# Performance work log

Measured on AMD Instinct MI355X. Metric: run time of the kernel, lower is better.

Reference implementation:

```python
import jax, jax.numpy as jnp
import numpy as np

N_NEIGHBORS = 200
OUT_HW = 64

def avg_pool3(x):
    # F.avg_pool2d(x, 3, stride=1, padding=1), count_include_pad=True -> divide by 9
    s = jax.lax.reduce_window(x, 0.0, jax.lax.add, (1, 1, 3, 3), (1, 1, 1, 1),
                              ((0, 0), (0, 0), (1, 1), (1, 1)))
    return s / 9.0

def coord_conv1x1(x, w, b):
    # CoordConv2d: append normalized x/y coord channels in [-1,1], then 1x1 conv.
    B, C, H, W = x.shape
    yy = jnp.linspace(-1.0, 1.0, H, dtype=x.dtype)
    xx = jnp.linspace(-1.0, 1.0, W, dtype=x.dtype)
    xg = jnp.broadcast_to(xx[None, :], (H, W))
    yg = jnp.broadcast_to(yy[:, None], (H, W))
    coords = jnp.broadcast_to(jnp.stack([xg, yg])[None], (B, 2, H, W))
    xc = jnp.concatenate([x, coords], axis=1)  # (B, C+2, H, W)
    return jnp.einsum('bchw,oc->bohw', xc, w) + b[None, :, None, None]

def resize64(x):
    B, C, _, _ = x.shape
    return jax.image.resize(x, (B, C, OUT_HW, OUT_HW), method='bilinear')

def descriptor(p0, p1, p2, w1, b1, w2, b2, w3, b3):
    o1 = resize64(coord_conv1x1(avg_pool3(p0), w1, b1))
    o2 = resize64(coord_conv1x1(avg_pool3(p1), w2, b2))
    o3 = resize64(coord_conv1x1(avg_pool3(p2), w3, b3))
    return jnp.concatenate([o1, o2, o3], axis=1)  # (B, 1792, 64, 64)

def setup_inputs() -> dict:
    key = jax.random.key(0)
    ks = jax.random.split(key, 10)
    s = 0.05
    return {
        'p0': jax.random.normal(ks[0], (4, 256, 64, 64), jnp.float32),
        'p1': jax.random.normal(ks[1], (4, 512, 32, 32), jnp.float32),
        'p2': jax.random.normal(ks[2], (4, 1024, 16, 16), jnp.float32),
        'label': 0,
        'mask': jnp.ones((4, 1, 64, 64), jnp.float32),
        'w1': jax.random.normal(ks[3], (256, 258), jnp.float32) * s,
        'b1': jax.random.normal(ks[4], (256,), jnp.float32) * s,
        'w2': jax.random.normal(ks[5], (512, 514), jnp.float32) * s,
        'b2': jax.random.normal(ks[6], (512,), jnp.float32) * s,
        'w3': jax.random.normal(ks[7], (1024, 1026), jnp.float32) * s,
        'b3': jax.random.normal(ks[8], (1024,), jnp.float32) * s,
        'C': jax.random.normal(ks[9], (1792, 4096), jnp.float32),
    }

def reference(p0, p1, p2, label, mask, w1, b1, w2, b2, w3, b3, C):
    PHI_P = descriptor(p0, p1, p2, w1, b1, w2, b2, w3, b3)  # (B, 1792, 64, 64)
    B = PHI_P.shape[0]
    # b c h w -> b (h w) c
    phi_p = PHI_P.reshape(B, 1792, OUT_HW * OUT_HW).transpose(0, 2, 1)  # (B, 4096, 1792)
    feats = jnp.sum(phi_p * phi_p, axis=2, keepdims=True)       # (B, 4096, 1)
    cents = jnp.sum(C * C, axis=0, keepdims=True)                # (1, 4096)
    f_c = 2.0 * jnp.matmul(phi_p, C)                             # (B, 4096, 4096)
    dist = jnp.sqrt(feats + cents - f_c)
    # topk smallest: top_k on negated distances, sorted ascending after negation
    neg_vals, _ = jax.lax.top_k(-dist, N_NEIGHBORS)              # (B, 4096, 200)
    score = -neg_vals
    # b (h w) c -> b c h w
    score = score.reshape(B, OUT_HW, OUT_HW, N_NEIGHBORS).transpose(0, 3, 1, 2)
    return (score, PHI_P[:, :896, :, :])
```

## Files before the change

### kernel.cpp

```cpp
#include <hip/hip_runtime.h>
#include <hip/hip_bf16.h>
#include <hip/hip_fp8.h>
#include <stdint.h>

typedef unsigned short u16;
typedef __attribute__((ext_vector_type(8))) short bf16x8;
typedef __attribute__((ext_vector_type(4))) unsigned short u16x4;
typedef __attribute__((ext_vector_type(4))) float f32x4;
typedef __attribute__((ext_vector_type(2))) long lx2;

#define AS1 __attribute__((address_space(1)))
#define AS3 __attribute__((address_space(3)))

__device__ __forceinline__ u16 f2bf(float f) {
  uint32_t x = __float_as_uint(f);
  uint32_t r = (x + 0x7FFFu + ((x >> 16) & 1u)) >> 16;
  return (u16)r;
}
__device__ __forceinline__ float bf2f(u16 u) {
  return __uint_as_float(((uint32_t)u) << 16);
}
__device__ __forceinline__ uint8_t f2f8(float f) {
  __hip_fp8_e4m3 t(f);
  return (uint8_t)t.__x;
}
__device__ __forceinline__ float f82f(uint8_t v) {
  __hip_fp8_e4m3 t;
  t.__x = (__hip_fp8_storage_t)v;
  return (float)t;
}

__device__ __forceinline__ int permcol(int c) {
  return (c & ~63) | (((c >> 3) & 3) << 4) | (((c >> 5) & 1) << 3) | (c & 7);
}

__device__ __forceinline__ void gload_lds16(const void* g, void* l) {
  __builtin_amdgcn_global_load_lds((const AS1 void*)g, (AS3 void*)l, 16, 0, 0);
}

template <int C, int H, int W>
__global__ __launch_bounds__(256) void pool_trans(const float* __restrict__ in,
                                                  u16* __restrict__ PT) {
  constexpr int HW = H * W;
  int hwt = blockIdx.x, ct = blockIdx.y, b = blockIdx.z;
  int tid = threadIdx.x;
  __shared__ float t[32][33];
  {
    int c_l = tid >> 3;
    int hw_l = (tid & 7) * 4;
    int c = ct * 32 + c_l;
    int hw = hwt * 32 + hw_l;
    int y = hw / W;
    int x0 = hw % W;
    const float* pl = in + ((size_t)b * C + c) * HW;
    float cs[6] = {0, 0, 0, 0, 0, 0};
    #pragma unroll
    for (int dy = -1; dy <= 1; dy++) {
      int yy = y + dy;
      if ((unsigned)yy < (unsigned)H) {
        const float* row = pl + yy * W;
        #pragma unroll
        for (int k = 0; k < 6; k++) {
          int xx = x0 - 1 + k;
          if ((unsigned)xx < (unsigned)W) cs[k] += row[xx];
        }
      }
    }
    #pragma unroll
    for (int k = 0; k < 4; k++)
      t[c_l][hw_l + k] = (cs[k] + cs[k + 1] + cs[k + 2]) * (1.0f / 9.0f);
  }
  __syncthreads();
  int hw_w = tid >> 3;
  int c_w = (tid & 7) * 4;
  u16x4 o;
  #pragma unroll
  for (int j = 0; j < 4; j++) o[j] = f2bf(t[c_w + j][hw_w]);
  *(u16x4*)&PT[((size_t)b * HW + hwt * 32 + hw_w) * C + ct * 32 + c_w] = o;
}

__global__ void wconv_bf16(const float* __restrict__ wf, u16* __restrict__ wb,
                           int logk, int total) {
  int idx = blockIdx.x * 256 + threadIdx.x;
  if (idx >= total) return;
  int K = 1 << logk;
  int o = idx >> (logk - 3);
  int k0 = (idx & ((K >> 3) - 1)) * 8;
  const float* src = wf + (size_t)o * (K + 2) + k0;
  bf16x8 v;
  #pragma unroll
  for (int e = 0; e < 8; e++) v[e] = (short)f2bf(src[e]);
  *(bf16x8*)&wb[(size_t)o * K + k0] = v;
}

template <int K, int HW, int WD, int OC, int PHIC, int CST, bool OUT8>
__global__ __launch_bounds__(256) void conv_gemm(
    const u16* __restrict__ Wb,
    const u16* __restrict__ PT,
    const float* __restrict__ wf,
    const float* __restrict__ bias,
    float* __restrict__ outHW, size_t outHW_bstride,
    void* __restrict__ outCM) {
  constexpr int LOGW = (WD == 64) ? 6 : (WD == 32) ? 5 : 4;
  constexpr int LOGHW = 2 * LOGW;
  int n0 = blockIdx.x * 128, m0 = blockIdx.y * 128;
  int tid = threadIdx.x;
  int wid = tid >> 6, lane = tid & 63;
  int wm = wid >> 1, wn = wid & 1;
  __shared__ u16 As[128 * 64];
  __shared__ u16 Bs[128 * 64];
  f32x4 acc[4][4] = {};
  int lrow = tid >> 3;
  int lcol = (tid & 7) * 8;
  const u16* ga = Wb + (size_t)(m0 + lrow) * K + lcol;
  const u16* gb = PT + (size_t)(n0 + lrow) * K + lcol;
  char* lbaseA = (char*)As + wid * 1024;
  char* lbaseB = (char*)Bs + wid * 1024;
  for (int k0 = 0; k0 < K; k0 += 64) {
    #pragma unroll
    for (int q = 0; q < 4; q++) {
      gload_lds16(ga + (size_t)q * 32 * K + k0, lbaseA + q * 4096);
      gload_lds16(gb + (size_t)q * 32 * K + k0, lbaseB + q * 4096);
    }
    __syncthreads();
    #pragma unroll
    for (int kk = 0; kk < 2; kk++) {
      bf16x8 af[4], bfr[4];
      int kb = kk * 32 + (lane >> 4) * 8;
      #pragma unroll
      for (int i = 0; i < 4; i++)
        af[i] = *(const bf16x8*)&As[(wm * 64 + i * 16 + (lane & 15)) * 64 + kb];
      #pragma unroll
      for (int j = 0; j < 4; j++)
        bfr[j] = *(const bf16x8*)&Bs[(wn * 64 + j * 16 + (lane & 15)) * 64 + kb];
      #pragma unroll
      for (int i = 0; i < 4; i++)
        #pragma unroll
        for (int j = 0; j < 4; j++)
          acc[i][j] = __builtin_amdgcn_mfma_f32_16x16x32_bf16(af[i], bfr[j], acc[i][j], 0, 0, 0);
    }
    __syncthreads();
  }
  int rq = lane >> 4, cq = lane & 15;
  #pragma unroll
  for (int mi = 0; mi < 4; mi++) {
    int lm = m0 + wm * 64 + mi * 16 + rq * 4;
    float wxr[4], wyr[4], bbr[4];
    #pragma unroll
    for (int r = 0; r < 4; r++) {
      int o = lm + r;
      wxr[r] = wf[(size_t)o * (K + 2) + K];
      wyr[r] = wf[(size_t)o * (K + 2) + K + 1];
      bbr[r] = bias[o];
    }
    #pragma unroll
    for (int ni = 0; ni < 4; ni++) {
      int gn = n0 + wn * 64 + ni * 16 + cq;
      int b = gn >> LOGHW;
      int hw = gn & (HW - 1);
      int x = hw & (WD - 1), y = hw >> LOGW;
      float xg = -1.0f + x * (2.0f / (WD - 1));
      float yg = -1.0f + y * (2.0f / (WD - 1));
      float vals[4];
      #pragma unroll
      for (int r = 0; r < 4; r++)
        vals[r] = acc[mi][ni][r] + wxr[r] * xg + wyr[r] * yg + bbr[r];
      if (lm < PHIC) {
        #pragma unroll
        for (int r = 0; r < 4; r++)
          outHW[(size_t)b * outHW_bstride + (size_t)(lm + r) * HW + hw] = vals[r];
      }
      if constexpr (OUT8) {
        uint32_t pk = (uint32_t)f2f8(vals[0]) | ((uint32_t)f2f8(vals[1]) << 8) |
                      ((uint32_t)f2f8(vals[2]) << 16) | ((uint32_t)f2f8(vals[3]) << 24);
        *(uint32_t*)&((uint8_t*)outCM)[((size_t)b * HW + hw) * CST + permcol(lm)] = pk;
      } else {
        u16x4 pk;
        #pragma unroll
        for (int r = 0; r < 4; r++) pk[r] = f2bf(vals[r]);
        *(u16x4*)&((u16*)outCM)[((size_t)b * HW + hw) * CST + lm] = pk;
      }
    }
  }
}

template <int Hin>
__device__ __forceinline__ void bilin_coords(int v, int& i0, int& i1, float& wgt) {
  constexpr float scale = (float)Hin / 64.0f;
  float f = ((float)v + 0.5f) * scale - 0.5f;
  float f0 = floorf(f);
  wgt = f - f0;
  int i = (int)f0;
  i1 = min(i + 1, Hin - 1);
  i0 = max(i, 0);
}

template <int C, int Cin, int Hin>
__global__ void emit_phi_v(const float* __restrict__ in, float* __restrict__ outp,
                           int ch_off) {
  int idx = blockIdx.x * 256 + threadIdx.x;
  int x0 = (idx & 15) * 4;
  int y = (idx >> 4) & 63;
  int c = (idx >> 10) % C;
  int b = idx / (C * 1024);
  const float* pl = in + (size_t)(b * Cin + c) * (Hin * Hin);
  int y0, y1; float wy;
  bilin_coords<Hin>(y, y0, y1, wy);
  const float* r0 = pl + y0 * Hin;
  const float* r1 = pl + y1 * Hin;
  f32x4 o;
  #pragma unroll
  for (int k = 0; k < 4; k++) {
    int xx0, xx1; float wx;
    bilin_coords<Hin>(x0 + k, xx0, xx1, wx);
    float top = (1.0f - wx) * r0[xx0] + wx * r0[xx1];
    float bot = (1.0f - wx) * r1[xx0] + wx * r1[xx1];
    o[k] = (1.0f - wy) * top + wy * bot;
  }
  *(f32x4*)&outp[((size_t)b * 896 + ch_off + c) * 4096 + (y << 6) + x0] = o;
}

__global__ __launch_bounds__(256) void trans_f32_fp8(
    const float* __restrict__ in, uint8_t* __restrict__ outT, int R, int Cc, int OS) {
  int r0 = blockIdx.y * 32, c0 = blockIdx.x * 32;
  __shared__ float t[32][33];
  int tid = threadIdx.x;
  int cl = tid & 31, rl = tid >> 5;
  #pragma unroll
  for (int q = 0; q < 4; q++)
    t[rl + q * 8][cl] = in[(size_t)(r0 + rl + q * 8) * Cc + c0 + cl];
  __syncthreads();
  #pragma unroll
  for (int q = 0; q < 4; q++) {
    int c = c0 + rl + q * 8;
    outT[(size_t)c * OS + permcol(r0 + cl)] = f2f8(t[cl][rl + q * 8]);
  }
}

template <int C, int Hin, int L>
__global__ void gather_A(const u16* __restrict__ OT, uint8_t* __restrict__ A,
                         int ch_off) {
  int idx = blockIdx.x * 256 + threadIdx.x;
  int co = (idx & ((C / 8) - 1)) * 8;
  int hw = (idx >> L) & 4095;
  int b = idx >> (L + 12);
  int x = hw & 63, y = hw >> 6;
  int y0, y1, x0, x1; float wy, wx;
  bilin_coords<Hin>(y, y0, y1, wy);
  bilin_coords<Hin>(x, x0, x1, wx);
  float w00 = (1.0f - wy) * (1.0f - wx), w01 = (1.0f - wy) * wx;
  float w10 = wy * (1.0f - wx), w11 = wy * wx;
  const u16* base = OT + (size_t)b * (Hin * Hin) * C + co;
  bf16x8 t00 = *(const bf16x8*)&base[(y0 * Hin + x0) * C];
  bf16x8 t01 = *(const bf16x8*)&base[(y0 * Hin + x1) * C];
  bf16x8 t10 = *(const bf16x8*)&base[(y1 * Hin + x0) * C];
  bf16x8 t11 = *(const bf16x8*)&base[(y1 * Hin + x1) * C];
  uint32_t pk[2] = {0, 0};
  #pragma unroll
  for (int e = 0; e < 8; e++) {
    float v = w00 * bf2f((u16)t00[e]) + w01 * bf2f((u16)t01[e]) +
              w10 * bf2f((u16)t10[e]) + w11 * bf2f((u16)t11[e]);
    pk[e >> 2] |= ((uint32_t)f2f8(v)) << ((e & 3) * 8);
  }
  uint2 o; o.x = pk[0]; o.y = pk[1];
  *(uint2*)&A[((size_t)b * 4096 + hw) * 1792 + permcol(ch_off + co)] = o;
}

__global__ __launch_bounds__(256) void rownorm8(const uint8_t* __restrict__ X,
                                                float* __restrict__ out, int ncols) {
  int row = blockIdx.x * 4 + (threadIdx.x >> 6);
  int lane = threadIdx.x & 63;
  const uint8_t* xr = X + (size_t)row * ncols;
  int n8 = ncols >> 3;
  float s = 0.0f;
  for (int c8 = lane; c8 < n8; c8 += 64) {
    uint2 v = *(const uint2*)&xr[c8 * 8];
    #pragma unroll
    for (int e = 0; e < 4; e++) {
      float f = f82f((uint8_t)((v.x >> (8 * e)) & 0xFF));
      s = fmaf(f, f, s);
    }
    #pragma unroll
    for (int e = 0; e < 4; e++) {
      float f = f82f((uint8_t)((v.y >> (8 * e)) & 0xFF));
      s = fmaf(f, f, s);
    }
  }
  #pragma unroll
  for (int off = 32; off; off >>= 1) s += __shfl_down(s, off);
  if (lane == 0) out[row] = s;
}

#define GD_NT 28

__device__ __forceinline__ void stage8k64(const uint8_t* __restrict__ G, int row0,
                                          int k0, char* lds_wavebase, int lane) {
  const int K = 1792;
  int sub = lane >> 2;
  int colsw = 16 * ((lane & 3) ^ ((lane >> 3) & 3));
  #pragma unroll
  for (int q = 0; q < 2; q++) {
    gload_lds16(G + (size_t)(row0 + q * 128 + sub) * K + k0 + colsw,
                lds_wavebase + q * 8192);
  }
}

__global__ __launch_bounds__(512, 2) void gemm_dist2(
    const uint8_t* __restrict__ A,
    const uint8_t* __restrict__ Bt,
    const float* __restrict__ feats, const float* __restrict__ cents,
    u16* __restrict__ S16, int m_base) {
  const int K = 1792, N = 4096;
  extern __shared__ uint8_t lds8[];
  int bid = blockIdx.x;
  int swz = (bid & 7) * 64 + (bid >> 3);
  int m0 = (swz >> 4) * 256;
  int n0 = (swz & 15) * 256;
  int tid = threadIdx.x;
  int wid = tid >> 6, lane = tid & 63;
  int wr = wid >> 2, wc = wid & 3;
  int ln15 = lane & 15;
  int fo = 16 * ((lane >> 4) ^ ((lane >> 1) & 3));

  f32x4 acc[8][4] = {};

  {
    char* bufb = (char*)lds8 + wid * 1024;
    stage8k64(A, m_base + m0 + wid * 16, 0, bufb, lane);
    stage8k64(Bt, n0 + wid * 16, 0, bufb + 16384, lane);
  }

  #pragma unroll 1
  for (int t = 0; t < GD_NT; t++) {
    asm volatile("s_waitcnt vmcnt(0)" ::: "memory");
    __builtin_amdgcn_s_barrier();
    __builtin_amdgcn_sched_barrier(0);
    const uint8_t* Ab = lds8 + (t & 1) * 32768;
    const uint8_t* Bb = Ab + 16384;
    char* nbuf = (char*)lds8 + ((t + 1) & 1) * 32768 + wid * 1024;

    lx2 bq[4], af[8];
    #pragma unroll
    for (int ni = 0; ni < 4; ni++)
      bq[ni] = *(const lx2*)&Bb[(wc * 64 + ni * 16 + ln15) * 64 + fo];
    #pragma unroll
    for (int mi = 0; mi < 8; mi++)
      af[mi] = *(const lx2*)&Ab[(wr * 128 + mi * 16 + ln15) * 64 + fo];

    if (t + 1 < GD_NT) {
      stage8k64(A, m_base + m0 + wid * 16, (t + 1) * 64, nbuf, lane);
      stage8k64(Bt, n0 + wid * 16, (t + 1) * 64, nbuf + 16384, lane);
    }

    __builtin_amdgcn_s_setprio(1);
    #pragma unroll
    for (int mi = 0; mi < 8; mi++)
      #pragma unroll
      for (int ni = 0; ni < 4; ni++)
        acc[mi][ni] = __builtin_amdgcn_mfma_f32_16x16x32_fp8_fp8(af[mi][0], bq[ni][0], acc[mi][ni], 0, 0, 0);
    #pragma unroll
    for (int mi = 0; mi < 8; mi++)
      #pragma unroll
      for (int ni = 0; ni < 4; ni++)
        acc[mi][ni] = __builtin_amdgcn_mfma_f32_16x16x32_fp8_fp8(af[mi][1], bq[ni][1], acc[mi][ni], 0, 0, 0);
    __builtin_amdgcn_s_setprio(0);
  }

  int rq = lane >> 4, cq = lane & 15;
  #pragma unroll
  for (int mi = 0; mi < 8; mi++) {
    int lm = m0 + wr * 128 + mi * 16 + rq * 4;
    #pragma unroll
    for (int ni = 0; ni < 4; ni++) {
      int gn = n0 + wc * 64 + ni * 16 + cq;
      float cn = cents[gn];
      #pragma unroll
      for (int r = 0; r < 4; r++)
        S16[(size_t)(lm + r) * N + gn] =
            f2bf(feats[m_base + lm + r] + cn - 2.0f * acc[mi][ni][r]);
    }
  }
}

__global__ __launch_bounds__(256) void select_topk(const u16* __restrict__ S16,
                                                   float* __restrict__ out,
                                                   int row_base) {
  int wv = threadIdx.x >> 6, lane = threadIdx.x & 63;
  int row_local = blockIdx.x * 4 + wv;
  const u16* Sr = S16 + (size_t)row_local * 4096;
  uint32_t ku[64];
  #pragma unroll
  for (int g = 0; g < 8; g++) {
    bf16x8 v = *(const bf16x8*)&Sr[g * 512 + lane * 8];
    #pragma unroll
    for (int e = 0; e < 8; e++) {
      uint32_t u = (uint32_t)(u16)v[e];
      u ^= (u & 0x8000u) ? 0xFFFFu : 0x8000u;
      ku[g * 8 + e] = u;
    }
  }
  uint32_t mn = 0xFFFFu, mx = 0u;
  #pragma unroll
  for (int j = 0; j < 64; j++) {
    mn = min(mn, ku[j]);
    mx = max(mx, ku[j]);
  }
  #pragma unroll
  for (int off = 1; off < 64; off <<= 1) {
    mn = min(mn, (uint32_t)__shfl_xor((int)mn, off));
    mx = max(mx, (uint32_t)__shfl_xor((int)mx, off));
  }
  uint32_t lo = mn, hi = mx;
  while (lo < hi) {
    uint32_t mid = (lo + hi) >> 1;
    int c = 0;
    #pragma unroll
    for (int j = 0; j < 64; j++) c += (ku[j] <= mid) ? 1 : 0;
    #pragma unroll
    for (int off = 1; off < 64; off <<= 1) c += __shfl_xor(c, off);
    if (c >= 200) hi = mid; else lo = mid + 1;
  }
  uint32_t T = lo;
  int cl = 0;
  #pragma unroll
  for (int j = 0; j < 64; j++) cl += (ku[j] < T) ? 1 : 0;
  int incl = cl;
  #pragma unroll
  for (int off = 1; off < 64; off <<= 1) {
    int v = __shfl_up(incl, off);
    if (lane >= off) incl += v;
  }
  int nless = __shfl(incl, 63);
  int pos = incl - cl;
  __shared__ uint32_t selv[4][256];
  uint32_t* sv = selv[wv];
  #pragma unroll
  for (int g = 0; g < 4; g++) sv[g * 64 + lane] = 0xFFFFFFFFu;
  for (int p = nless + lane; p < 200; p += 64) sv[p] = T;
  #pragma unroll
  for (int j = 0; j < 64; j++)
    if (ku[j] < T) sv[pos++] = ku[j];
  uint32_t v[4];
  #pragma unroll
  for (int q = 0; q < 4; q++) v[q] = sv[q * 64 + lane];
  #pragma unroll
  for (int kk = 2; kk <= 256; kk <<= 1) {
    #pragma unroll
    for (int jj = kk >> 1; jj > 0; jj >>= 1) {
      if (jj >= 64) {
        int qb = jj >> 6;
        #pragma unroll
        for (int q = 0; q < 4; q++) {
          if ((q & qb) == 0) {
            int q2 = q | qb;
            bool up = (kk == 256) ? true : ((q & (kk >> 6)) == 0);
            uint32_t a = v[q], b2 = v[q2];
            uint32_t lo2 = min(a, b2), hi2 = max(a, b2);
            v[q] = up ? lo2 : hi2;
            v[q2] = up ? hi2 : lo2;
          }
        }
      } else {
        #pragma unroll
        for (int q = 0; q < 4; q++) {
          bool up;
          if (kk == 256) up = true;
          else if (kk == 128) up = ((q & 2) == 0);
          else if (kk == 64) up = ((q & 1) == 0);
          else up = ((lane & kk) == 0);
          uint32_t other = (uint32_t)__shfl_xor((int)v[q], jj);
          bool lower = ((lane & jj) == 0);
          uint32_t lo2 = min(v[q], other), hi2 = max(v[q], other);
          v[q] = (up == lower) ? lo2 : hi2;
        }
      }
    }
  }
  int grow = row_base + row_local;
  int b = grow >> 12, r = grow & 4095;
  #pragma unroll
  for (int q = 0; q < 4; q++) {
    int i = q * 64 + lane;
    if (i < 200) {
      uint32_t u = v[q] & 0xFFFFu;
      u ^= (u & 0x8000u) ? 0x8000u : 0xFFFFu;
      out[((size_t)b * 200 + i) * 4096 + r] = sqrtf(bf2f((u16)u));
    }
  }
}

extern "C" void kernel_launch(void* const* d_in, const int* in_sizes, int n_in,
                              void* d_out, int out_size, void* d_ws, size_t ws_size,
                              hipStream_t stream) {
  const float* p0 = (const float*)d_in[0];
  const float* p1 = (const float*)d_in[1];
  const float* p2 = (const float*)d_in[2];
  const float* w1 = (const float*)d_in[5];
  const float* b1 = (const float*)d_in[6];
  const float* w2 = (const float*)d_in[7];
  const float* b2 = (const float*)d_in[8];
  const float* w3 = (const float*)d_in[9];
  const float* b3 = (const float*)d_in[10];
  const float* Cm = (const float*)d_in[11];

  float* out_score = (float*)d_out;
  float* out_phi = (float*)d_out + 3276800;

  char* w = (char*)d_ws;
  uint8_t* A8 = (uint8_t*)w;
  uint8_t* Ct8 = (uint8_t*)(w + 29360128);
  float* feats = (float*)(w + 36700160);
  float* cents = (float*)(w + 36765696);
  u16* S16 = (u16*)(w + 36782080);
  u16* PT1 = (u16*)(w + 36782080);
  u16* PT2 = (u16*)(w + 45170688);
  u16* PT3 = (u16*)(w + 49364992);
  u16* Wbf1 = (u16*)(w + 51462144);
  u16* Wbf2 = (u16*)(w + 51593216);
  u16* Wbf3 = (u16*)(w + 52117504);
  float* O2 = (float*)(w + 54214656);
  float* O3 = (float*)(w + 62603264);
  u16* OT2 = (u16*)(w + 63127552);
  u16* OT3 = (u16*)(w + 67321856);

  pool_trans<256, 64, 64><<<dim3(128, 8, 4), 256, 0, stream>>>(p0, PT1);
  pool_trans<512, 32, 32><<<dim3(32, 16, 4), 256, 0, stream>>>(p1, PT2);
  pool_trans<1024, 16, 16><<<dim3(8, 32, 4), 256, 0, stream>>>(p2, PT3);

  wconv_bf16<<<32, 256, 0, stream>>>(w1, Wbf1, 8, 8192);
  wconv_bf16<<<128, 256, 0, stream>>>(w2, Wbf2, 9, 32768);
  wconv_bf16<<<512, 256, 0, stream>>>(w3, Wbf3, 10, 131072);

  conv_gemm<256, 4096, 64, 256, 256, 1792, true><<<dim3(128, 2), 256, 0, stream>>>(
      Wbf1, PT1, w1, b1, out_phi, (size_t)896 * 4096, A8);
  conv_gemm<512, 1024, 32, 512, 512, 512, false><<<dim3(32, 4), 256, 0, stream>>>(
      Wbf2, PT2, w2, b2, O2, (size_t)512 * 1024, OT2);
  conv_gemm<1024, 256, 16, 1024, 128, 1024, false><<<dim3(8, 8), 256, 0, stream>>>(
      Wbf3, PT3, w3, b3, O3, (size_t)128 * 256, OT3);

  emit_phi_v<512, 512, 32><<<8192, 256, 0, stream>>>(O2, out_phi, 256);
  emit_phi_v<128, 128, 16><<<2048, 256, 0, stream>>>(O3, out_phi, 768);

  gather_A<512, 32, 6><<<4096, 256, 0, stream>>>(OT2, A8, 256);
  gather_A<1024, 16, 7><<<8192, 256, 0, stream>>>(OT3, A8, 768);

  trans_f32_fp8<<<dim3(128, 56), 256, 0, stream>>>(Cm, Ct8, 1792, 4096, 1792);

  rownorm8<<<4096, 256, 0, stream>>>(A8, feats, 1792);
  rownorm8<<<1024, 256, 0, stream>>>(Ct8, cents, 1792);

  for (int mc = 0; mc < 2; mc++) {
    gemm_dist2<<<512, 512, 65536, stream>>>(A8, Ct8, feats, cents, S16, mc * 8192);
    select_topk<<<2048, 256, 0, stream>>>(S16, out_score, mc * 8192);
  }
}
```

Before: 388.4 us.

## Shrink distance GEMM block tile to 256x128 with four waves per block

The fp8 distance GEMM drops from 256x256 tiles with 8 waves to 256x128 tiles with 4 waves, so each wave still owns a 128x64 output subtile. Staging is split into separate A (four 64-row chunks) and B (two chunks) loaders, the double-buffered LDS shrinks from 64 KB to 48 KB, and the grid doubles to 1024 blocks with a matching swizzle. The aim is more blocks and better occupancy or load balance across CUs, at the cost of more redundant global reads of A per output.

```diff
diff --git a/kernel.cpp b/kernel.cpp
--- a/kernel.cpp
+++ b/kernel.cpp
@@ -293,19 +293,26 @@
 
 #define GD_NT 28
 
-__device__ __forceinline__ void stage8k64(const uint8_t* __restrict__ G, int row0,
-                                          int k0, char* lds_wavebase, int lane) {
+__device__ __forceinline__ void stageA2(const uint8_t* __restrict__ G, int row0,
+                                        int k0, char* dest, int lane) {
   const int K = 1792;
   int sub = lane >> 2;
   int colsw = 16 * ((lane & 3) ^ ((lane >> 3) & 3));
   #pragma unroll
-  for (int q = 0; q < 2; q++) {
-    gload_lds16(G + (size_t)(row0 + q * 128 + sub) * K + k0 + colsw,
-                lds_wavebase + q * 8192);
-  }
-}
-
-__global__ __launch_bounds__(512, 2) void gemm_dist2(
+  for (int q = 0; q < 4; q++)
+    gload_lds16(G + (size_t)(row0 + q * 64 + sub) * K + k0 + colsw, dest + q * 4096);
+}
+__device__ __forceinline__ void stageB2(const uint8_t* __restrict__ G, int row0,
+                                        int k0, char* dest, int lane) {
+  const int K = 1792;
+  int sub = lane >> 2;
+  int colsw = 16 * ((lane & 3) ^ ((lane >> 3) & 3));
+  #pragma unroll
+  for (int q = 0; q < 2; q++)
+    gload_lds16(G + (size_t)(row0 + q * 64 + sub) * K + k0 + colsw, dest + q * 4096);
+}
+
+__global__ __launch_bounds__(256, 2) void gemm_dist2(
     const uint8_t* __restrict__ A,
     const uint8_t* __restrict__ Bt,
     const float* __restrict__ feats, const float* __restrict__ cents,
@@ -313,31 +320,28 @@
   const int K = 1792, N = 4096;
   extern __shared__ uint8_t lds8[];
   int bid = blockIdx.x;
-  int swz = (bid & 7) * 64 + (bid >> 3);
-  int m0 = (swz >> 4) * 256;
-  int n0 = (swz & 15) * 256;
+  int swz = (bid & 7) * 128 + (bid >> 3);
+  int m0 = (swz >> 5) * 256;
+  int n0 = (swz & 31) * 128;
   int tid = threadIdx.x;
   int wid = tid >> 6, lane = tid & 63;
-  int wr = wid >> 2, wc = wid & 3;
+  int wr = wid >> 1, wc = wid & 1;
   int ln15 = lane & 15;
   int fo = 16 * ((lane >> 4) ^ ((lane >> 1) & 3));
 
   f32x4 acc[8][4] = {};
 
-  {
-    char* bufb = (char*)lds8 + wid * 1024;
-    stage8k64(A, m_base + m0 + wid * 16, 0, bufb, lane);
-    stage8k64(Bt, n0 + wid * 16, 0, bufb + 16384, lane);
-  }
+  stageA2(A, m_base + m0 + wid * 16, 0, (char*)lds8 + wid * 1024, lane);
+  stageB2(Bt, n0 + wid * 16, 0, (char*)lds8 + 16384 + wid * 1024, lane);
 
   #pragma unroll 1
   for (int t = 0; t < GD_NT; t++) {
     asm volatile("s_waitcnt vmcnt(0)" ::: "memory");
     __builtin_amdgcn_s_barrier();
     __builtin_amdgcn_sched_barrier(0);
-    const uint8_t* Ab = lds8 + (t & 1) * 32768;
+    const uint8_t* Ab = lds8 + (t & 1) * 24576;
     const uint8_t* Bb = Ab + 16384;
-    char* nbuf = (char*)lds8 + ((t + 1) & 1) * 32768 + wid * 1024;
+    char* nb = (char*)lds8 + ((t + 1) & 1) * 24576;
 
     lx2 bq[4], af[8];
     #pragma unroll
@@ -348,8 +352,8 @@
       af[mi] = *(const lx2*)&Ab[(wr * 128 + mi * 16 + ln15) * 64 + fo];
 
     if (t + 1 < GD_NT) {
-      stage8k64(A, m_base + m0 + wid * 16, (t + 1) * 64, nbuf, lane);
-      stage8k64(Bt, n0 + wid * 16, (t + 1) * 64, nbuf + 16384, lane);
+      stageA2(A, m_base + m0 + wid * 16, (t + 1) * 64, nb + wid * 1024, lane);
+      stageB2(Bt, n0 + wid * 16, (t + 1) * 64, nb + 16384 + wid * 1024, lane);
     }
 
     __builtin_amdgcn_s_setprio(1);
@@ -550,7 +554,7 @@
   rownorm8<<<1024, 256, 0, stream>>>(Ct8, cents, 1792);
 
   for (int mc = 0; mc < 2; mc++) {
-    gemm_dist2<<<512, 512, 65536, stream>>>(A8, Ct8, feats, cents, S16, mc * 8192);
+    gemm_dist2<<<1024, 256, 49152, stream>>>(A8, Ct8, feats, cents, S16, mc * 8192);
     select_topk<<<2048, 256, 0, stream>>>(S16, out_score, mc * 8192);
   }
 }
```

Result: no change. 382.0 us (-1.7%).
